# Kernel optimization log

Measured on AMD Instinct MI355X. Metric: run time of the kernel, lower is better.

The kernel has to match this reference:

```python
import jax, jax.numpy as jnp
import numpy as np

NEG_INF = -1e9


def _gru_cell(x, h, W_ih, W_hh, b_ih, b_hh):
    # torch GRUCell math, gate order [r; z; n]
    gx = x @ W_ih.T + b_ih          # [B, 3H]
    gh = h @ W_hh.T + b_hh          # [B, 3H]
    xr, xz, xn = jnp.split(gx, 3, axis=-1)
    hr, hz, hn = jnp.split(gh, 3, axis=-1)
    r = jax.nn.sigmoid(xr + hr)
    z = jax.nn.sigmoid(xz + hz)
    n = jnp.tanh(xn + r * hn)
    return (1.0 - z) * n + z * h


def setup_inputs() -> dict:
    key = jax.random.key(0)
    ks = jax.random.split(key, 8)
    B, N, D, H, P = 64, 2048, 256, 256, 256
    s = 0.05
    return {
        "sequence": jax.random.normal(ks[0], (B, N, D), jnp.float32),
        "hidden_t": jax.random.normal(ks[1], (B, H), jnp.float32),
        "sequence_mask": jnp.ones((B, N), jnp.float32),
        "num_steps": 2,
        "W_seq": jax.random.normal(ks[2], (D, P), jnp.float32) * s,
        "W_h": jax.random.normal(ks[3], (H, P), jnp.float32) * s,
        "v_att": jax.random.normal(ks[4], (P,), jnp.float32) * s,
        "W_ih": jax.random.normal(ks[5], (3 * H, D), jnp.float32) * s,
        "W_hh": jax.random.normal(ks[6], (3 * H, H), jnp.float32) * s,
        "b_ih": jnp.zeros((3 * H,), jnp.float32),
        "b_hh": jnp.zeros((3 * H,), jnp.float32),
    }


def reference(sequence, hidden_t, sequence_mask, num_steps,
              W_seq, W_h, v_att, W_ih, W_hh, b_ih, b_hh):
    # Precompute the sequence projection once (invariant across decode steps).
    seq_proj = jnp.einsum("bnd,dp->bnp", sequence, W_seq)   # [B, N, P]
    mask_bias = jnp.where(sequence_mask > 0, 0.0, NEG_INF)  # [B, N]

    def step(h, _):
        # projection similarity: v . tanh(W1 s_i + W2 h)
        proj = jnp.tanh(seq_proj + (h @ W_h)[:, None, :])   # [B, N, P]
        scores = jnp.einsum("bnp,p->bn", proj, v_att) + mask_bias
        w = jax.nn.softmax(scores, axis=-1)                  # [B, N]
        vec = jnp.einsum("bn,bnd->bd", w, sequence)          # [B, D]
        h_new = _gru_cell(vec, h, W_ih, W_hh, b_ih, b_hh)
        return h_new, w

    _, ws = jax.lax.scan(step, hidden_t, None, length=num_steps)  # [T, B, N]
    return jnp.transpose(ws, (1, 0, 2))                            # [B, T, N]
```

## Files before the change

kernel.cpp:

```cpp
#include <hip/hip_runtime.h>
#include <cstdint>

using u16 = unsigned short;
using u32 = unsigned int;
typedef __attribute__((ext_vector_type(8))) short bf16x8;
typedef __attribute__((ext_vector_type(8))) u16 u16x8;
typedef __attribute__((ext_vector_type(16))) float f32x16;
typedef __attribute__((ext_vector_type(2))) u32 u32x2;
typedef __attribute__((ext_vector_type(4))) u32 u32x4;

#define DEV static __device__ __forceinline__

DEV u16 bf16_rne(float x) {
  u32 u = __float_as_uint(x);
  u32 r = (u + 0x7FFFu + ((u >> 16) & 1u)) >> 16;
  return (u16)r;
}
DEV float bf16f(u16 h) { return __uint_as_float(((u32)h) << 16); }

DEV u32 cvt_pk_bf16(float lo, float hi) {
  u32 d;
  asm("v_cvt_pk_bf16_f32 %0, %1, %2" : "=v"(d) : "v"(lo), "v"(hi));
  return d;
}

DEV float fast_tanh(float x) {
  float e = __expf(2.0f * x);
  return fmaf(-2.0f, __builtin_amdgcn_rcpf(e + 1.0f), 1.0f);
}
DEV float sigmoidf_(float x) {
  return __builtin_amdgcn_rcpf(1.0f + __expf(-x));
}

__global__ __launch_bounds__(256) void prep_w(const float* __restrict__ Wseq,
                                              const float* __restrict__ Wih,
                                              const float* __restrict__ Whh,
                                              u16* __restrict__ WfG,
                                              float* __restrict__ WT,
                                              float* __restrict__ UT) {
  const int bid = blockIdx.x, t = threadIdx.x;
  if (bid < 32) {
    const int unit = bid * 4 + (t >> 6);
    const int lane = t & 63, l31 = lane & 31, koct = lane >> 5;
    const int pt8 = unit >> 4, kt = unit & 15;
    u16x8 o;
#pragma unroll
    for (int e = 0; e < 8; ++e)
      o[e] = bf16_rne(
          Wseq[(long)(kt * 16 + koct * 8 + e) * 256 + pt8 * 32 + l31]);
    *(u16x8*)(WfG + (long)unit * 512 + lane * 8) = o;
  } else {
    const int gid = bid - 32;
    const float* src = (gid >= 12) ? Whh : Wih;
    float* dst = (gid >= 12) ? UT : WT;
    const int g = (gid % 12) * 64 + (t & 63);
    const int dq = t >> 6;
#pragma unroll 4
    for (int d = dq * 64; d < dq * 64 + 64; ++d)
      dst[(long)d * 768 + g] = src[(long)g * 256 + d];
  }
}

__global__ __launch_bounds__(256) void hw_q(const float* __restrict__ h,
                                            const float* __restrict__ Wh,
                                            float* __restrict__ hw) {
  const int q = blockIdx.x, b = blockIdx.y, t = threadIdx.x;
  __shared__ float sh[256];
  __shared__ float sP[4][64];
  sh[t] = h[b * 256 + t];
  __syncthreads();
  const int j4 = t & 63, dg = t >> 6;
  const int j = q * 64 + j4;
  float g = 0.f;
#pragma unroll 4
  for (int k = dg * 64; k < dg * 64 + 64; ++k)
    g = fmaf(sh[k], Wh[(long)k * 256 + j], g);
  sP[dg][j4] = g;
  __syncthreads();
  if (t < 64)
    hw[b * 256 + q * 64 + t] = (sP[0][t] + sP[1][t]) + (sP[2][t] + sP[3][t]);
}

struct EpiSmem {
  float sQ[128][5];
  float se[128];
  float shw[256];
  float svv[256];
  float sredE[2];
};

template <bool FROMLDS>
DEV void epilogue(EpiSmem& sm, const f32x16& a00, const f32x16& a01,
                  const f32x16& a10, const f32x16& a11, const u16* bs,
                  const char* sRb, const float* __restrict__ mask,
                  float* __restrict__ wbuf, float* __restrict__ esum,
                  float* __restrict__ part, long nbase, int esumIdx,
                  long partBase, int t, int lane, int w, int l31, int koct,
                  int pg, int ng) {
  float s0a = 0.f, s0b = 0.f, s0c = 0.f, s0d = 0.f;
  float s1a = 0.f, s1b = 0.f, s1c = 0.f, s1d = 0.f;
#pragma unroll
  for (int r = 0; r < 16; r += 4) {
    const int c0 = (r & 3) + 8 * (r >> 2) + 4 * koct;
    const int c1 = ((r + 1) & 3) + 8 * ((r + 1) >> 2) + 4 * koct;
    const int c2 = ((r + 2) & 3) + 8 * ((r + 2) >> 2) + 4 * koct;
    const int c3 = ((r + 3) & 3) + 8 * ((r + 3) >> 2) + 4 * koct;
    const int p0 = pg * 64 + c0, p1 = pg * 64 + c1, p2 = pg * 64 + c2,
              p3 = pg * 64 + c3;
    s0a = fmaf(sm.svv[p0], fast_tanh(a00[r] + sm.shw[p0]), s0a);
    s0b = fmaf(sm.svv[p1], fast_tanh(a00[r + 1] + sm.shw[p1]), s0b);
    s0c = fmaf(sm.svv[p2], fast_tanh(a00[r + 2] + sm.shw[p2]), s0c);
    s0d = fmaf(sm.svv[p3], fast_tanh(a00[r + 3] + sm.shw[p3]), s0d);
    s1a = fmaf(sm.svv[p0], fast_tanh(a01[r] + sm.shw[p0]), s1a);
    s1b = fmaf(sm.svv[p1], fast_tanh(a01[r + 1] + sm.shw[p1]), s1b);
    s1c = fmaf(sm.svv[p2], fast_tanh(a01[r + 2] + sm.shw[p2]), s1c);
    s1d = fmaf(sm.svv[p3], fast_tanh(a01[r + 3] + sm.shw[p3]), s1d);
  }
#pragma unroll
  for (int r = 0; r < 16; r += 4) {
    const int c0 = (r & 3) + 8 * (r >> 2) + 4 * koct;
    const int c1 = ((r + 1) & 3) + 8 * ((r + 1) >> 2) + 4 * koct;
    const int c2 = ((r + 2) & 3) + 8 * ((r + 2) >> 2) + 4 * koct;
    const int c3 = ((r + 3) & 3) + 8 * ((r + 3) >> 2) + 4 * koct;
    const int p0 = pg * 64 + 32 + c0, p1 = pg * 64 + 32 + c1,
              p2 = pg * 64 + 32 + c2, p3 = pg * 64 + 32 + c3;
    s0a = fmaf(sm.svv[p0], fast_tanh(a10[r] + sm.shw[p0]), s0a);
    s0b = fmaf(sm.svv[p1], fast_tanh(a10[r + 1] + sm.shw[p1]), s0b);
    s0c = fmaf(sm.svv[p2], fast_tanh(a10[r + 2] + sm.shw[p2]), s0c);
    s0d = fmaf(sm.svv[p3], fast_tanh(a10[r + 3] + sm.shw[p3]), s0d);
    s1a = fmaf(sm.svv[p0], fast_tanh(a11[r] + sm.shw[p0]), s1a);
    s1b = fmaf(sm.svv[p1], fast_tanh(a11[r + 1] + sm.shw[p1]), s1b);
    s1c = fmaf(sm.svv[p2], fast_tanh(a11[r + 2] + sm.shw[p2]), s1c);
    s1d = fmaf(sm.svv[p3], fast_tanh(a11[r + 3] + sm.shw[p3]), s1d);
  }
  float sc0 = (s0a + s0b) + (s0c + s0d);
  float sc1 = (s1a + s1b) + (s1c + s1d);
  sc0 += __shfl_xor(sc0, 32, 64);
  sc1 += __shfl_xor(sc1, 32, 64);
  if (koct == 0) {
    sm.sQ[ng * 64 + l31][pg] = sc0;
    sm.sQ[ng * 64 + 32 + l31][pg] = sc1;
  }
  __syncthreads();
  if (t < 128) {
    float s = (sm.sQ[t][0] + sm.sQ[t][1]) + (sm.sQ[t][2] + sm.sQ[t][3]);
    const long n = nbase + t;
    float e = (mask[n] > 0.f) ? __expf(s) : 0.f;
    sm.se[t] = e;
    wbuf[n] = e;
    float s4 = e;
#pragma unroll
    for (int off = 1; off < 64; off <<= 1) s4 += __shfl_xor(s4, off, 64);
    if ((t & 63) == 0) sm.sredE[t >> 6] = s4;
  }
  __syncthreads();
  if (t == 0) esum[esumIdx] = sm.sredE[0] + sm.sredE[1];

#pragma unroll
  for (int kk = 0; kk < 2; ++kk) {
    const int kt = w + kk * 8;
    float vd0 = 0, vd1 = 0, vd2 = 0, vd3 = 0, vd4 = 0, vd5 = 0, vd6 = 0,
          vd7 = 0;
#pragma unroll
    for (int t8 = 0; t8 < 4; ++t8) {
      u16x8 q;
      if constexpr (FROMLDS) {
        const int row = t8 * 32 + l31;
        const int colb = (kt * 16 + koct * 8) * 2;
        q = *(const u16x8*)(sRb + row * 512 + (colb ^ ((row & 31) << 4)));
      } else {
        q = *(const u16x8*)(bs + ((long)(t8 * 16 + kt) * 64 + lane) * 8);
      }
      const float wv = sm.se[t8 * 32 + l31];
      vd0 = fmaf(wv, bf16f((u16)q[0]), vd0);
      vd1 = fmaf(wv, bf16f((u16)q[1]), vd1);
      vd2 = fmaf(wv, bf16f((u16)q[2]), vd2);
      vd3 = fmaf(wv, bf16f((u16)q[3]), vd3);
      vd4 = fmaf(wv, bf16f((u16)q[4]), vd4);
      vd5 = fmaf(wv, bf16f((u16)q[5]), vd5);
      vd6 = fmaf(wv, bf16f((u16)q[6]), vd6);
      vd7 = fmaf(wv, bf16f((u16)q[7]), vd7);
    }
#pragma unroll
    for (int off = 1; off < 32; off <<= 1) {
      vd0 += __shfl_xor(vd0, off, 64);
      vd1 += __shfl_xor(vd1, off, 64);
      vd2 += __shfl_xor(vd2, off, 64);
      vd3 += __shfl_xor(vd3, off, 64);
      vd4 += __shfl_xor(vd4, off, 64);
      vd5 += __shfl_xor(vd5, off, 64);
      vd6 += __shfl_xor(vd6, off, 64);
      vd7 += __shfl_xor(vd7, off, 64);
    }
    if (l31 == 0) {
      float4 o0 = {vd0, vd1, vd2, vd3};
      float4 o1 = {vd4, vd5, vd6, vd7};
      float* pp = part + partBase * 256 + kt * 16 + koct * 8;
      *(float4*)pp = o0;
      *(float4*)(pp + 4) = o1;
    }
  }
}

__global__ __launch_bounds__(512, 4) void step0k(
    const float* __restrict__ seq, u16* __restrict__ seqF,
    const u16* __restrict__ WfG, const float* __restrict__ hwbuf,
    const float* __restrict__ vatt, const float* __restrict__ mask,
    float* __restrict__ wbuf, float* __restrict__ esum,
    float* __restrict__ part, int N, int NCH2, int B) {
  __shared__ __align__(16) u16 sR[32768];
  __shared__ EpiSmem sm;

  const int t = threadIdx.x, lane = t & 63, w = t >> 6;
  const int l31 = lane & 31, koct = lane >> 5;
  const int pg = w >> 1, ng = w & 1;
  const int b = blockIdx.y, ch = blockIdx.x;
  char* sRb = (char*)sR;
  const long chbase = (long)(b * NCH2 + ch) << 15;

  const u16* wa0 = WfG + (long)(pg * 32) * 512 + lane * 8;
  const u16* wa1 = wa0 + 8192;
  u16x8 w00 = *(const u16x8*)(wa0 + 0 * 512);
  u16x8 w01 = *(const u16x8*)(wa1 + 0 * 512);
  u16x8 w10 = *(const u16x8*)(wa0 + 1 * 512);
  u16x8 w11 = *(const u16x8*)(wa1 + 1 * 512);
  u16x8 w20 = *(const u16x8*)(wa0 + 2 * 512);
  u16x8 w21 = *(const u16x8*)(wa1 + 2 * 512);
  u16x8 w30 = *(const u16x8*)(wa0 + 3 * 512);
  u16x8 w31 = *(const u16x8*)(wa1 + 3 * 512);

  {
    const float* src = seq + ((long)b * N + ch * 128) * 256;
#pragma unroll
    for (int i = 0; i < 16; ++i) {
      const int idx = i * 2048 + t * 4;
      float4 x = *(const float4*)(src + idx);
      u32x2 o;
      o[0] = cvt_pk_bf16(x.x, x.y);
      o[1] = cvt_pk_bf16(x.z, x.w);
      const int row = idx >> 8, colb = (idx & 255) * 2;
      *(u32x2*)(sRb + row * 512 + (colb ^ ((row & 31) << 4))) = o;
    }
  }
  if (t < 256) {
    sm.shw[t] = hwbuf[b * 256 + t];
    sm.svv[t] = vatt[t];
  }
  __syncthreads();

  {
    u16* dst = seqF + chbase;
#pragma unroll
    for (int i = 0; i < 8; ++i) {
      const int uidx = i * 512 + t;
      const int ln = uidx & 63, unit = uidx >> 6;
      const int kt = unit & 15, t8 = unit >> 4;
      const int row = t8 * 32 + (ln & 31);
      const int colb = (kt * 16 + (ln >> 5) * 8) * 2;
      u16x8 v = *(const u16x8*)(sRb + row * 512 + (colb ^ ((row & 31) << 4)));
      *(u16x8*)(dst + (long)uidx * 8) = v;
    }
  }

  f32x16 a00 = (f32x16)0.f, a01 = (f32x16)0.f, a10 = (f32x16)0.f,
         a11 = (f32x16)0.f;
  {
    const int row0 = ng * 64 + l31, row1 = row0 + 32;
    const char* p0 = sRb + row0 * 512;
    const char* p1 = sRb + row1 * 512;
    const int sw0 = (row0 & 31) << 4, sw1 = (row1 & 31) << 4;
    const int cb = koct * 16;
#define MFMA4W(AF0, AF1, kt)                                                   \
  {                                                                            \
    bf16x8 bf0 = *(const bf16x8*)(p0 + (((kt) * 32 + cb) ^ sw0));              \
    bf16x8 bf1 = *(const bf16x8*)(p1 + (((kt) * 32 + cb) ^ sw1));              \
    a00 = __builtin_amdgcn_mfma_f32_32x32x16_bf16(AF0, bf0, a00, 0, 0, 0);     \
    a01 = __builtin_amdgcn_mfma_f32_32x32x16_bf16(AF0, bf1, a01, 0, 0, 0);     \
    a10 = __builtin_amdgcn_mfma_f32_32x32x16_bf16(AF1, bf0, a10, 0, 0, 0);     \
    a11 = __builtin_amdgcn_mfma_f32_32x32x16_bf16(AF1, bf1, a11, 0, 0, 0);     \
  }
    MFMA4W(*(bf16x8*)&w00, *(bf16x8*)&w01, 0);
    MFMA4W(*(bf16x8*)&w10, *(bf16x8*)&w11, 1);
    MFMA4W(*(bf16x8*)&w20, *(bf16x8*)&w21, 2);
    MFMA4W(*(bf16x8*)&w30, *(bf16x8*)&w31, 3);
#pragma unroll 4
    for (int kt = 4; kt < 16; ++kt) {
      bf16x8 af0 = *(const bf16x8*)(wa0 + kt * 512);
      bf16x8 af1 = *(const bf16x8*)(wa1 + kt * 512);
      MFMA4W(af0, af1, kt);
    }
#undef MFMA4W
  }
  __syncthreads();
  epilogue<true>(sm, a00, a01, a10, a11, nullptr, sRb, mask, wbuf, esum, part,
                 (long)b * N + ch * 128, b * NCH2 + ch, (long)ch * B + b, t,
                 lane, w, l31, koct, pg, ng);
}

__global__ __launch_bounds__(512, 4) void step1k(
    const u16* __restrict__ seqF, const u16* __restrict__ WfG,
    const float* __restrict__ hwbuf, const float* __restrict__ vatt,
    const float* __restrict__ mask, float* __restrict__ wbuf,
    float* __restrict__ esum, float* __restrict__ part, int N, int NCH2,
    int B) {
  __shared__ EpiSmem sm;
  const int t = threadIdx.x, lane = t & 63, w = t >> 6;
  const int l31 = lane & 31, koct = lane >> 5;
  const int pg = w >> 1, ng = w & 1;
  const int b = blockIdx.y, ch = blockIdx.x;
  const long chbase = (long)(b * NCH2 + ch) << 15;

  if (t < 256) {
    sm.shw[t] = hwbuf[b * 256 + t];
    sm.svv[t] = vatt[t];
  }

  const u16* bs0 = seqF + chbase + ng * 16384 + lane * 8;
  const u16* bs1 = bs0 + 8192;
  const u16* wa0 = WfG + (long)(pg * 32) * 512 + lane * 8;
  const u16* wa1 = wa0 + 8192;

  f32x16 a00 = (f32x16)0.f, a01 = (f32x16)0.f, a10 = (f32x16)0.f,
         a11 = (f32x16)0.f;

  u16x8 A0c, A1c, B0c, B1c, A0n, A1n, B0n, B1n;
  A0c = *(const u16x8*)(wa0);
  A1c = *(const u16x8*)(wa1);
  B0c = *(const u16x8*)(bs0);
  B1c = *(const u16x8*)(bs1);

#define MFMA4(A0, A1, B0, B1)                                                  \
  {                                                                            \
    bf16x8 af0 = *(bf16x8*)&A0, af1 = *(bf16x8*)&A1;                           \
    bf16x8 bf0 = *(bf16x8*)&B0, bf1 = *(bf16x8*)&B1;                           \
    a00 = __builtin_amdgcn_mfma_f32_32x32x16_bf16(af0, bf0, a00, 0, 0, 0);     \
    a01 = __builtin_amdgcn_mfma_f32_32x32x16_bf16(af0, bf1, a01, 0, 0, 0);     \
    a10 = __builtin_amdgcn_mfma_f32_32x32x16_bf16(af1, bf0, a10, 0, 0, 0);     \
    a11 = __builtin_amdgcn_mfma_f32_32x32x16_bf16(af1, bf1, a11, 0, 0, 0);     \
  }

#pragma unroll
  for (int kt2 = 0; kt2 < 8; ++kt2) {
    const int kn = kt2 * 2 + 1;
    A0n = *(const u16x8*)(wa0 + kn * 512);
    A1n = *(const u16x8*)(wa1 + kn * 512);
    B0n = *(const u16x8*)(bs0 + kn * 512);
    B1n = *(const u16x8*)(bs1 + kn * 512);
    MFMA4(A0c, A1c, B0c, B1c);
    if (kt2 < 7) {
      const int kc = kt2 * 2 + 2;
      A0c = *(const u16x8*)(wa0 + kc * 512);
      A1c = *(const u16x8*)(wa1 + kc * 512);
      B0c = *(const u16x8*)(bs0 + kc * 512);
      B1c = *(const u16x8*)(bs1 + kc * 512);
    }
    MFMA4(A0n, A1n, B0n, B1n);
  }
#undef MFMA4

  __syncthreads();
  epilogue<false>(sm, a00, a01, a10, a11, seqF + chbase, nullptr, mask, wbuf,
                  esum, part, (long)b * N + ch * 128, b * NCH2 + ch,
                  (long)ch * B + b, t, lane, w, l31, koct, pg, ng);
}

__global__ __launch_bounds__(256) void finalize_gru(
    const float* __restrict__ part, const float* __restrict__ esumP, int ecnt,
    const float* __restrict__ hprev, const float* __restrict__ WT,
    const float* __restrict__ UT, const float* __restrict__ bih,
    const float* __restrict__ bhh, const float* __restrict__ wbuf,
    float* __restrict__ out, float* __restrict__ hnew, int N, int T, int step,
    int NP, int B) {
  const int q = blockIdx.x, b = blockIdx.y, t = threadIdx.x;
  __shared__ float sv[256], sh[256], sP[6][4][64];
  float S = 0.f;
  for (int i = 0; i < ecnt; ++i) S += esumP[b * ecnt + i];
  const float inv = __builtin_amdgcn_rcpf(S);
  float a = 0.f;
  for (int cc = 0; cc < NP; ++cc) a += part[((long)cc * B + b) * 256 + t];
  sv[t] = a * inv;
  sh[t] = hprev[b * 256 + t];
  __syncthreads();
  const int j4 = t & 63, dg = t >> 6;
  const int j = q * 64 + j4;
  float g0 = 0, g1 = 0, g2 = 0, g3 = 0, g4 = 0, g5 = 0;
#pragma unroll 4
  for (int d = dg * 64; d < dg * 64 + 64; ++d) {
    const float vd = sv[d], hd = sh[d];
    const float* wr_ = WT + (long)d * 768 + j;
    const float* ur_ = UT + (long)d * 768 + j;
    g0 = fmaf(vd, wr_[0], g0);
    g1 = fmaf(vd, wr_[256], g1);
    g2 = fmaf(vd, wr_[512], g2);
    g3 = fmaf(hd, ur_[0], g3);
    g4 = fmaf(hd, ur_[256], g4);
    g5 = fmaf(hd, ur_[512], g5);
  }
  sP[0][dg][j4] = g0;
  sP[1][dg][j4] = g1;
  sP[2][dg][j4] = g2;
  sP[3][dg][j4] = g3;
  sP[4][dg][j4] = g4;
  sP[5][dg][j4] = g5;
  __syncthreads();
  if (t < 64) {
    const int jj = q * 64 + t;
    float xr = bih[jj], xz = bih[256 + jj], xn = bih[512 + jj];
    float hr = bhh[jj], hz = bhh[256 + jj], hn = bhh[512 + jj];
#pragma unroll
    for (int dgg = 0; dgg < 4; ++dgg) {
      xr += sP[0][dgg][t];
      xz += sP[1][dgg][t];
      xn += sP[2][dgg][t];
      hr += sP[3][dgg][t];
      hz += sP[4][dgg][t];
      hn += sP[5][dgg][t];
    }
    float rr = sigmoidf_(xr + hr);
    float zz = sigmoidf_(xz + hz);
    float nn = fast_tanh(xn + rr * hn);
    hnew[b * 256 + jj] = (1.f - zz) * nn + zz * sh[jj];
  }
  const long ob = ((long)b * T + step) * N;
  const int nq = N >> 2;
  for (int i = 0; i * 256 < nq; ++i) {
    const int n = q * nq + i * 256 + t;
    out[ob + n] = wbuf[(long)b * N + n] * inv;
  }
}

extern "C" void kernel_launch(void* const* d_in, const int* in_sizes, int n_in,
                              void* d_out, int out_size, void* d_ws,
                              size_t ws_size, hipStream_t stream) {
  (void)n_in;
  (void)ws_size;
  const float* seq = (const float*)d_in[0];
  const float* hidden = (const float*)d_in[1];
  const float* mask = (const float*)d_in[2];
  const float* Wseq = (const float*)d_in[4];
  const float* Wh = (const float*)d_in[5];
  const float* vatt = (const float*)d_in[6];
  const float* Wih = (const float*)d_in[7];
  const float* Whh = (const float*)d_in[8];
  const float* bih = (const float*)d_in[9];
  const float* bhh = (const float*)d_in[10];
  float* out = (float*)d_out;

  const int P = in_sizes[6];
  const int H = in_sizes[5] / P;
  const int B = in_sizes[1] / H;
  const int N = in_sizes[2] / B;
  const int T = out_size / (B * N);
  const long M = (long)B * N;
  const int NCH2 = N / 128;

  char* p = (char*)d_ws;
  auto alloc = [&](size_t bytes) {
    char* r = p;
    p += (bytes + 255) & ~(size_t)255;
    return r;
  };
  u16* seqF = (u16*)alloc((size_t)M * 256 * 2);
  u16* WfG = (u16*)alloc((size_t)256 * 256 * 2);
  float* WT = (float*)alloc((size_t)256 * 768 * 4);
  float* UT = (float*)alloc((size_t)256 * 768 * 4);
  float* wbuf = (float*)alloc((size_t)B * N * 4);
  float* hwbuf = (float*)alloc((size_t)B * 256 * 4);
  float* hA = (float*)alloc((size_t)B * 256 * 4);
  float* hB = (float*)alloc((size_t)B * 256 * 4);
  float* part = (float*)alloc((size_t)NCH2 * B * 256 * 4);
  float* esum = (float*)alloc((size_t)B * NCH2 * 4);
  float* hbuf[2] = {hA, hB};

  prep_w<<<dim3(56), dim3(256), 0, stream>>>(Wseq, Wih, Whh, WfG, WT, UT);

  for (int t = 0; t < T; ++t) {
    const float* hcur = (t == 0) ? hidden : hbuf[(t - 1) & 1];
    hw_q<<<dim3(4, B), dim3(256), 0, stream>>>(hcur, Wh, hwbuf);
    if (t == 0) {
      step0k<<<dim3(NCH2, B), dim3(512), 0, stream>>>(
          seq, seqF, WfG, hwbuf, vatt, mask, wbuf, esum, part, N, NCH2, B);
    } else {
      step1k<<<dim3(NCH2, B), dim3(512), 0, stream>>>(
          seqF, WfG, hwbuf, vatt, mask, wbuf, esum, part, N, NCH2, B);
    }
    finalize_gru<<<dim3(4, B), dim3(256), 0, stream>>>(
        part, esum, NCH2, hcur, WT, UT, bih, bhh, wbuf, out, hbuf[t & 1], N, T,
        t, NCH2, B);
  }
}
```

Baseline: 146.3 us.

## Process two chunks per step0 block, overlapping next fill with epilogue

The step-0 kernel now handles two 128-row chunks per block, halving the grid. The second chunk's global load and bf16 conversion into shared memory are issued before the first chunk's epilogue, which reads from the global bf16 copy instead of shared memory, so the load can overlap epilogue work. Launch bounds drop from 4 to 2 blocks per CU, and the weight-register prefetch of the first four k-tiles is removed. Risks include lower occupancy and the epilogue reading global memory just written by the same block.

```diff
diff --git a/kernel.cpp b/kernel.cpp
--- a/kernel.cpp
+++ b/kernel.cpp
@@ -202,7 +202,7 @@
   }
 }
 
-__global__ __launch_bounds__(512, 4) void step0k(
+__global__ __launch_bounds__(512, 2) void step0k(
     const float* __restrict__ seq, u16* __restrict__ seqF,
     const u16* __restrict__ WfG, const float* __restrict__ hwbuf,
     const float* __restrict__ vatt, const float* __restrict__ mask,
@@ -214,22 +214,11 @@
   const int t = threadIdx.x, lane = t & 63, w = t >> 6;
   const int l31 = lane & 31, koct = lane >> 5;
   const int pg = w >> 1, ng = w & 1;
-  const int b = blockIdx.y, ch = blockIdx.x;
+  const int b = blockIdx.y;
+  const int c0 = blockIdx.x * 2, c1 = c0 + 1;
   char* sRb = (char*)sR;
-  const long chbase = (long)(b * NCH2 + ch) << 15;
-
-  const u16* wa0 = WfG + (long)(pg * 32) * 512 + lane * 8;
-  const u16* wa1 = wa0 + 8192;
-  u16x8 w00 = *(const u16x8*)(wa0 + 0 * 512);
-  u16x8 w01 = *(const u16x8*)(wa1 + 0 * 512);
-  u16x8 w10 = *(const u16x8*)(wa0 + 1 * 512);
-  u16x8 w11 = *(const u16x8*)(wa1 + 1 * 512);
-  u16x8 w20 = *(const u16x8*)(wa0 + 2 * 512);
-  u16x8 w21 = *(const u16x8*)(wa1 + 2 * 512);
-  u16x8 w30 = *(const u16x8*)(wa0 + 3 * 512);
-  u16x8 w31 = *(const u16x8*)(wa1 + 3 * 512);
-
-  {
+
+  auto fill = [&](int ch) {
     const float* src = seq + ((long)b * N + ch * 128) * 256;
 #pragma unroll
     for (int i = 0; i < 16; ++i) {
@@ -241,15 +230,9 @@
       const int row = idx >> 8, colb = (idx & 255) * 2;
       *(u32x2*)(sRb + row * 512 + (colb ^ ((row & 31) << 4))) = o;
     }
-  }
-  if (t < 256) {
-    sm.shw[t] = hwbuf[b * 256 + t];
-    sm.svv[t] = vatt[t];
-  }
-  __syncthreads();
-
-  {
-    u16* dst = seqF + chbase;
+  };
+  auto writeout = [&](int ch) {
+    u16* dst = seqF + ((long)(b * NCH2 + ch) << 15);
 #pragma unroll
     for (int i = 0; i < 8; ++i) {
       const int uidx = i * 512 + t;
@@ -260,40 +243,53 @@
       u16x8 v = *(const u16x8*)(sRb + row * 512 + (colb ^ ((row & 31) << 4)));
       *(u16x8*)(dst + (long)uidx * 8) = v;
     }
-  }
-
-  f32x16 a00 = (f32x16)0.f, a01 = (f32x16)0.f, a10 = (f32x16)0.f,
-         a11 = (f32x16)0.f;
-  {
+  };
+  const u16* wa0 = WfG + (long)(pg * 32) * 512 + lane * 8;
+  const u16* wa1 = wa0 + 8192;
+  auto gemm = [&](f32x16& a00, f32x16& a01, f32x16& a10, f32x16& a11) {
     const int row0 = ng * 64 + l31, row1 = row0 + 32;
     const char* p0 = sRb + row0 * 512;
     const char* p1 = sRb + row1 * 512;
     const int sw0 = (row0 & 31) << 4, sw1 = (row1 & 31) << 4;
     const int cb = koct * 16;
-#define MFMA4W(AF0, AF1, kt)                                                   \
-  {                                                                            \
-    bf16x8 bf0 = *(const bf16x8*)(p0 + (((kt) * 32 + cb) ^ sw0));              \
-    bf16x8 bf1 = *(const bf16x8*)(p1 + (((kt) * 32 + cb) ^ sw1));              \
-    a00 = __builtin_amdgcn_mfma_f32_32x32x16_bf16(AF0, bf0, a00, 0, 0, 0);     \
-    a01 = __builtin_amdgcn_mfma_f32_32x32x16_bf16(AF0, bf1, a01, 0, 0, 0);     \
-    a10 = __builtin_amdgcn_mfma_f32_32x32x16_bf16(AF1, bf0, a10, 0, 0, 0);     \
-    a11 = __builtin_amdgcn_mfma_f32_32x32x16_bf16(AF1, bf1, a11, 0, 0, 0);     \
-  }
-    MFMA4W(*(bf16x8*)&w00, *(bf16x8*)&w01, 0);
-    MFMA4W(*(bf16x8*)&w10, *(bf16x8*)&w11, 1);
-    MFMA4W(*(bf16x8*)&w20, *(bf16x8*)&w21, 2);
-    MFMA4W(*(bf16x8*)&w30, *(bf16x8*)&w31, 3);
 #pragma unroll 4
-    for (int kt = 4; kt < 16; ++kt) {
+    for (int kt = 0; kt < 16; ++kt) {
       bf16x8 af0 = *(const bf16x8*)(wa0 + kt * 512);
       bf16x8 af1 = *(const bf16x8*)(wa1 + kt * 512);
-      MFMA4W(af0, af1, kt);
-    }
-#undef MFMA4W
-  }
-  __syncthreads();
-  epilogue<true>(sm, a00, a01, a10, a11, nullptr, sRb, mask, wbuf, esum, part,
-                 (long)b * N + ch * 128, b * NCH2 + ch, (long)ch * B + b, t,
+      bf16x8 bf0 = *(const bf16x8*)(p0 + ((kt * 32 + cb) ^ sw0));
+      bf16x8 bf1 = *(const bf16x8*)(p1 + ((kt * 32 + cb) ^ sw1));
+      a00 = __builtin_amdgcn_mfma_f32_32x32x16_bf16(af0, bf0, a00, 0, 0, 0);
+      a01 = __builtin_amdgcn_mfma_f32_32x32x16_bf16(af0, bf1, a01, 0, 0, 0);
+      a10 = __builtin_amdgcn_mfma_f32_32x32x16_bf16(af1, bf0, a10, 0, 0, 0);
+      a11 = __builtin_amdgcn_mfma_f32_32x32x16_bf16(af1, bf1, a11, 0, 0, 0);
+    }
+  };
+
+  fill(c0);
+  if (t < 256) {
+    sm.shw[t] = hwbuf[b * 256 + t];
+    sm.svv[t] = vatt[t];
+  }
+  __syncthreads();
+  writeout(c0);
+  f32x16 a00 = (f32x16)0.f, a01 = (f32x16)0.f, a10 = (f32x16)0.f,
+         a11 = (f32x16)0.f;
+  gemm(a00, a01, a10, a11);
+  __syncthreads();
+
+  fill(c1);
+  epilogue<false>(sm, a00, a01, a10, a11,
+                  seqF + ((long)(b * NCH2 + c0) << 15), nullptr, mask, wbuf,
+                  esum, part, (long)b * N + c0 * 128, b * NCH2 + c0,
+                  (long)c0 * B + b, t, lane, w, l31, koct, pg, ng);
+
+  writeout(c1);
+  f32x16 b00 = (f32x16)0.f, b01 = (f32x16)0.f, b10 = (f32x16)0.f,
+         b11 = (f32x16)0.f;
+  gemm(b00, b01, b10, b11);
+  __syncthreads();
+  epilogue<true>(sm, b00, b01, b10, b11, nullptr, sRb, mask, wbuf, esum, part,
+                 (long)b * N + c1 * 128, b * NCH2 + c1, (long)c1 * B + b, t,
                  lane, w, l31, koct, pg, ng);
 }
 
@@ -478,7 +474,7 @@
     const float* hcur = (t == 0) ? hidden : hbuf[(t - 1) & 1];
     hw_q<<<dim3(4, B), dim3(256), 0, stream>>>(hcur, Wh, hwbuf);
     if (t == 0) {
-      step0k<<<dim3(NCH2, B), dim3(512), 0, stream>>>(
+      step0k<<<dim3(NCH2 / 2, B), dim3(512), 0, stream>>>(
           seq, seqF, WfG, hwbuf, vatt, mask, wbuf, esum, part, N, NCH2, B);
     } else {
       step1k<<<dim3(NCH2, B), dim3(512), 0, stream>>>(
```

New measurement: 167.3 us. +14.4%, slower.
